# Performance work log

Hardware: AMD Instinct MI355X
Metric: run time of the kernel (lower is better)

## Reference

```python
import jax, jax.numpy as jnp
import numpy as np

N, E = 20000, 320000
NODE_DIM, EDGE_DIM, EMB, HEADS, HIDDEN, OUT = 128, 16, 128, 4, 512, 64
NEG_SLOPE = 0.2


def _gatv2(x, src0, dst0, ea, Wl, bl, Wr, br, We, att, bias):
    """PyG GATv2Conv (concat=True, add_self_loops=True, fill_value='mean')."""
    n = x.shape[0]
    e = src0.shape[0]
    H, C = att.shape
    # self loops; self-loop edge_attr = mean of incoming edge_attr per node (0 if none)
    cnt = jax.ops.segment_sum(jnp.ones((e,), x.dtype), dst0, num_segments=n)
    loop_attr = jax.ops.segment_sum(ea, dst0, num_segments=n) / jnp.maximum(cnt, 1.0)[:, None]
    loops = jnp.arange(n, dtype=src0.dtype)
    src = jnp.concatenate([src0, loops])
    dst = jnp.concatenate([dst0, loops])
    ea_full = jnp.concatenate([ea, loop_attr], axis=0)
    xl = (x @ Wl + bl).reshape(n, H, C)   # source transform
    xr = (x @ Wr + br).reshape(n, H, C)   # target transform
    ef = (ea_full @ We).reshape(-1, H, C)  # edge transform (no bias in PyG)
    s = jax.nn.leaky_relu(xl[src] + xr[dst] + ef, NEG_SLOPE)  # [E', H, C]
    logits = jnp.einsum('ehc,hc->eh', s, att)
    # scatter-softmax over incoming edges of each dst node (stable)
    mx = jax.ops.segment_max(logits, dst, num_segments=n)
    num = jnp.exp(logits - mx[dst])
    den = jax.ops.segment_sum(num, dst, num_segments=n)
    alpha = num / (den[dst] + 1e-16)
    out = jax.ops.segment_sum(alpha[:, :, None] * xl[src], dst, num_segments=n)
    return out.reshape(n, H * C) + bias


def _lin(key, fan_in, fan_out, dt=jnp.float32):
    return jax.random.normal(key, (fan_in, fan_out), dt) * (1.0 / np.sqrt(fan_in))


def setup_inputs() -> dict:
    key = jax.random.key(0)
    ks = jax.random.split(key, 24)
    HC = HEADS * EMB
    inp = {
        'x': jax.random.normal(ks[0], (N, NODE_DIM), jnp.float32),
        'edge_index': jax.random.randint(ks[1], (2, E), 0, N, jnp.int64),
        'edge_attr': jax.random.normal(ks[2], (E, EDGE_DIM), jnp.float32),
        # GATv2 layer 1
        'Wl1': _lin(ks[3], NODE_DIM, HC), 'bl1': jnp.zeros((HC,), jnp.float32),
        'Wr1': _lin(ks[4], NODE_DIM, HC), 'br1': jnp.zeros((HC,), jnp.float32),
        'We1': _lin(ks[5], EDGE_DIM, HC),
        'att1': jax.random.normal(ks[6], (HEADS, EMB), jnp.float32) * (1.0 / np.sqrt(EMB)),
        'bias1': jnp.zeros((HC,), jnp.float32),
        # GATv2 layer 2
        'Wl2': _lin(ks[7], HC, HC), 'bl2': jnp.zeros((HC,), jnp.float32),
        'Wr2': _lin(ks[8], HC, HC), 'br2': jnp.zeros((HC,), jnp.float32),
        'We2': _lin(ks[9], EDGE_DIM, HC),
        'att2': jax.random.normal(ks[10], (HEADS, EMB), jnp.float32) * (1.0 / np.sqrt(EMB)),
        'bias2': jnp.zeros((HC,), jnp.float32),
        # decoder MLP
        'Wd1': _lin(ks[11], HC, HIDDEN), 'bd1': jnp.zeros((HIDDEN,), jnp.float32),
        'Wd2': _lin(ks[12], HIDDEN, OUT), 'bd2': jnp.zeros((OUT,), jnp.float32),
    }
    return inp


def reference(x, edge_index, edge_attr,
              Wl1, bl1, Wr1, br1, We1, att1, bias1,
              Wl2, bl2, Wr2, br2, We2, att2, bias2,
              Wd1, bd1, Wd2, bd2):
    src, dst = edge_index[0], edge_index[1]
    h = _gatv2(x, src, dst, edge_attr, Wl1, bl1, Wr1, br1, We1, att1, bias1)
    h = _gatv2(h, src, dst, edge_attr, Wl2, bl2, Wr2, br2, We2, att2, bias2)
    q = jax.nn.relu(h @ Wd1 + bd1) @ Wd2 + bd2
    return q
```

## Files before the change

### kernel.cpp

```cpp
#include <hip/hip_runtime.h>
#include <hip/hip_fp16.h>

typedef _Float16 half8 __attribute__((ext_vector_type(8)));
typedef _Float16 half4 __attribute__((ext_vector_type(4)));
typedef _Float16 half2v __attribute__((ext_vector_type(2)));
typedef float f32x4 __attribute__((ext_vector_type(4)));

#if __has_builtin(__builtin_amdgcn_fdot2)
#define FDOT2(a, b, c) __builtin_amdgcn_fdot2((a), (b), (c), false)
#else
static __device__ __forceinline__ float FDOT2(half2v a, half2v b, float c) {
  return (float)a[0] * (float)b[0] + (float)a[1] * (float)b[1] + c;
}
#endif
#define H2(v8, p) ((half2v){(v8)[2 * (p)], (v8)[2 * (p) + 1]})

#define GLOAD_LDS16(gp, lp)                                                        \
  __builtin_amdgcn_global_load_lds(                                                \
      (const __attribute__((address_space(1))) void*)(gp),                         \
      (__attribute__((address_space(3))) void*)(lp), 16, 0, 0)

template <int CTRL>
__device__ __forceinline__ float dpp_add16(float x) {
  int y = __builtin_amdgcn_update_dpp(0, __float_as_int(x), CTRL, 0xf, 0xf, true);
  return x + __int_as_float(y);
}
__device__ __forceinline__ float rowsum16(float x) {
  x = dpp_add16<0x128>(x);
  x = dpp_add16<0x124>(x);
  x = dpp_add16<0x122>(x);
  x = dpp_add16<0x121>(x);
  return x;
}

__device__ __forceinline__ int xcd_remap(int bid, int nwg) {
  int xcd = bid & 7, idx = bid >> 3;
  int q8 = nwg >> 3, r8 = nwg & 7;
  return (xcd < r8) ? (xcd * (q8 + 1) + idx)
                    : (r8 * (q8 + 1) + (xcd - r8) * q8 + idx);
}

__global__ void prep_kernel(const float* __restrict__ x, _Float16* __restrict__ x16, int nx,
                            const float* __restrict__ Wl1, const float* __restrict__ Wr1,
                            _Float16* __restrict__ WlrT1,
                            const float* __restrict__ Wl2, const float* __restrict__ Wr2,
                            _Float16* __restrict__ WlrT2,
                            const float* __restrict__ Wd1, _Float16* __restrict__ WdT1,
                            const float* __restrict__ Wd2, _Float16* __restrict__ WdT2,
                            const float* __restrict__ We1, _Float16* __restrict__ WeF1,
                            const float* __restrict__ We2, _Float16* __restrict__ WeF2,
                            const float* __restrict__ att1, _Float16* __restrict__ att16_1,
                            const float* __restrict__ att2, _Float16* __restrict__ att16_2,
                            const int* __restrict__ dst0, int* __restrict__ deg, int E) {
  int i = blockIdx.x * 256 + threadIdx.x;
  if (i < nx) { x16[i] = (_Float16)x[i]; return; }
  i -= nx;
  if (i < 1024 * 128) {
    int n = i >> 7, k = i & 127;
    float v = (n < 512) ? Wl1[(size_t)k * 512 + n] : Wr1[(size_t)k * 512 + (n - 512)];
    WlrT1[i] = (_Float16)v; return;
  }
  i -= 1024 * 128;
  if (i < 1024 * 512) {
    int n = i >> 9, k = i & 511;
    float v = (n < 512) ? Wl2[(size_t)k * 512 + n] : Wr2[(size_t)k * 512 + (n - 512)];
    WlrT2[i] = (_Float16)v; return;
  }
  i -= 1024 * 512;
  if (i < 512 * 512) { int n = i >> 9, k = i & 511; WdT1[i] = (_Float16)Wd1[(size_t)k * 512 + n]; return; }
  i -= 512 * 512;
  if (i < 64 * 512)  { int n = i >> 9, k = i & 511; WdT2[i] = (_Float16)Wd2[(size_t)k * 64 + n]; return; }
  i -= 64 * 512;
  if (i < 512 * 16) {
    int k = i & 15, c = (i >> 4) & 15, g = i >> 8;
    WeF1[i] = (_Float16)We1[(size_t)k * 512 + g * 16 + c]; return;
  }
  i -= 512 * 16;
  if (i < 512 * 16) {
    int k = i & 15, c = (i >> 4) & 15, g = i >> 8;
    WeF2[i] = (_Float16)We2[(size_t)k * 512 + g * 16 + c]; return;
  }
  i -= 512 * 16;
  if (i < 512)       { att16_1[i] = (_Float16)att1[i]; return; }
  i -= 512;
  if (i < 512)       { att16_2[i] = (_Float16)att2[i]; return; }
  i -= 512;
  if (i < E)         { atomicAdd(&deg[dst0[i]], 1); return; }
}

__global__ __launch_bounds__(1024) void scan_kernel(const int* __restrict__ deg, int* __restrict__ offs, int N) {
  __shared__ int part[1024];
  int t = threadIdx.x;
  int chunk = (N + 1023) / 1024;
  int b = t * chunk, e = min(b + chunk, N);
  int s = 0;
  for (int i = b; i < e; i++) s += deg[i] + 1;
  part[t] = s;
  __syncthreads();
  for (int off = 1; off < 1024; off <<= 1) {
    int v = (t >= off) ? part[t - off] : 0;
    __syncthreads();
    part[t] += v;
    __syncthreads();
  }
  int run = (t == 0) ? 0 : part[t - 1];
  for (int i = b; i < e; i++) { offs[i] = run; run += deg[i] + 1; }
  if (t == 1023) offs[N] = part[1023];
}

__global__ void csr_fill_kernel(const int* __restrict__ src0, const int* __restrict__ dst0,
                                const float* __restrict__ ea,
                                const int* __restrict__ offs, const int* __restrict__ deg,
                                int* __restrict__ cnt, int* __restrict__ csr_src,
                                _Float16* __restrict__ eas, int E, int N) {
  int i = blockIdx.x * 256 + threadIdx.x;
  if (i < 64) {
    if (i < 16) csr_src[E + N + i] = 0;
#pragma unroll
    for (int k = 0; k < 16; k++) eas[(size_t)(E + N + i) * 16 + k] = (_Float16)0.f;
  }
  if (i < E) {
    int d = dst0[i];
    int p = offs[d] + atomicAdd(&cnt[d], 1);
    csr_src[p] = src0[i];
    const float* s = ea + (size_t)i * 16;
    half8 h0, h1;
#pragma unroll
    for (int k = 0; k < 8; k++) { h0[k] = (_Float16)s[k]; h1[k] = (_Float16)s[k + 8]; }
    *(half8*)(eas + (size_t)p * 16) = h0;
    *(half8*)(eas + (size_t)p * 16 + 8) = h1;
  } else if (i < E + N) {
    int v = i - E;
    csr_src[offs[v] + deg[v]] = v;
  }
}

__global__ void loop_attr_kernel(const int* __restrict__ offs, const int* __restrict__ deg,
                                 _Float16* __restrict__ eas, int N) {
  int wid = (blockIdx.x * 256 + threadIdx.x) >> 6;
  int l = threadIdx.x & 63;
  if (wid >= N) return;
  int b = offs[wid], dg = deg[wid];
  int k = l & 15, r = l >> 4;
  float s = 0.f;
  for (int j = r; j < dg; j += 4)
    s += (float)eas[(size_t)(b + j) * 16 + k];
  s += __shfl_xor(s, 16, 64);
  s += __shfl_xor(s, 32, 64);
  if (r == 0) eas[(size_t)(b + dg) * 16 + k] = (_Float16)(s / fmaxf((float)dg, 1.0f));
}

template <bool RELU, bool OUT_F32>
__global__ __launch_bounds__(256) void gemm_f16(const _Float16* __restrict__ A,
                                                const _Float16* __restrict__ BT,
                                                const float* __restrict__ biasA,
                                                const float* __restrict__ biasB,
                                                void* __restrict__ CA,
                                                void* __restrict__ CB,
                                                int M, int K, int Nfull, int ldc) {
  __shared__ _Float16 SBUF[4 * 64 * 64];
  _Float16* As = SBUF;
  _Float16* Bs = SBUF + 4096;
  int t = threadIdx.x;
  int gx = gridDim.x, gy = gridDim.y;
  int nwg = gx * gy;
  int bid2 = xcd_remap(blockIdx.y * gx + blockIdx.x, nwg);
  int m0 = (bid2 / gy) * 128;
  int n0 = (bid2 % gy) * 128;
  int l = t & 63, w = t >> 6;
  int wm = w & 1, wn = w >> 1;
  int lr = l & 15, lq = l >> 4;

  f32x4 acc[4][4];
#pragma unroll
  for (int i = 0; i < 4; i++)
#pragma unroll
    for (int j = 0; j < 4; j++) acc[i][j] = (f32x4){0.f, 0.f, 0.f, 0.f};

  int r0 = w * 32 + (l >> 2);
  int cb = (l & 3) * 8;
  const _Float16* Ap = A + (size_t)(m0 + r0) * K + cb;
  const _Float16* Bp = BT + (size_t)(n0 + r0) * K + cb;
  _Float16* AsW = As + w * 32 * 32;
  _Float16* BsW = Bs + w * 32 * 32;

  for (int kk = 0; kk < K; kk += 32) {
    GLOAD_LDS16(Ap, AsW);
    GLOAD_LDS16(Ap + (size_t)16 * K, AsW + 16 * 32);
    GLOAD_LDS16(Bp, BsW);
    GLOAD_LDS16(Bp + (size_t)16 * K, BsW + 16 * 32);
    Ap += 32; Bp += 32;
    __syncthreads();
    half8 af[4], bf[4];
#pragma unroll
    for (int mi = 0; mi < 4; mi++) af[mi] = *(const half8*)&As[(wm * 64 + mi * 16 + lr) * 32 + lq * 8];
#pragma unroll
    for (int ni = 0; ni < 4; ni++) bf[ni] = *(const half8*)&Bs[(wn * 64 + ni * 16 + lr) * 32 + lq * 8];
#pragma unroll
    for (int mi = 0; mi < 4; mi++)
#pragma unroll
      for (int ni = 0; ni < 4; ni++)
        acc[mi][ni] = __builtin_amdgcn_mfma_f32_16x16x32_f16(af[mi], bf[ni], acc[mi][ni], 0, 0, 0);
    __syncthreads();
  }

  if (!OUT_F32) {
    int colbase = n0 + wn * 64;
    const float* biasP = (colbase < 512) ? biasA : biasB;
    int cb0 = (colbase < 512) ? colbase : colbase - 512;
    _Float16* Cx = (_Float16*)((colbase < 512) ? CA : CB);
    _Float16* Cw = SBUF + w * 4096;
#pragma unroll
    for (int ni = 0; ni < 4; ni++) {
      float bv = biasP[cb0 + ni * 16 + lr];
#pragma unroll
      for (int mi = 0; mi < 4; mi++) {
#pragma unroll
        for (int r = 0; r < 4; r++) {
          float v = acc[mi][ni][r] + bv;
          if (RELU) v = fmaxf(v, 0.f);
          Cw[(mi * 16 + lq * 4 + r) * 64 + ni * 16 + lr] = (_Float16)v;
        }
      }
    }
    __syncthreads();
    int lrow = l >> 3, lcb = (l & 7) * 8;
#pragma unroll
    for (int ps = 0; ps < 8; ps++) {
      int row = m0 + wm * 64 + ps * 8 + lrow;
      half8 vv = *(const half8*)(Cw + (ps * 8 + lrow) * 64 + lcb);
      if (row < M) *(half8*)(Cx + (size_t)row * ldc + cb0 + lcb) = vv;
    }
  } else {
#pragma unroll
    for (int ni = 0; ni < 4; ni++) {
      int col = n0 + wn * 64 + ni * 16 + lr;
      if (col >= Nfull) continue;
      float bv = (col < 512) ? biasA[col] : biasB[col - 512];
      float* Cx = (float*)((col < 512) ? CA : CB);
      int cc = (col < 512) ? col : col - 512;
#pragma unroll
      for (int mi = 0; mi < 4; mi++) {
#pragma unroll
        for (int r = 0; r < 4; r++) {
          int row = m0 + wm * 64 + mi * 16 + lq * 4 + r;
          if (row >= M) continue;
          float v = acc[mi][ni][r] + bv;
          if (RELU) v = fmaxf(v, 0.f);
          Cx[(size_t)row * ldc + cc] = v;
        }
      }
    }
  }
}


__device__ __forceinline__ void upd(float p, half8 xs, float& m, float& den, float acc[8]) {
  float mn = fmaxf(m, p);
  float sc = __expf(m - mn);
  float al = __expf(p - mn);
  den = den * sc + al;
#pragma unroll
  for (int jj = 0; jj < 8; jj++) acc[jj] = acc[jj] * sc + al * (float)xs[jj];
  m = mn;
}

__global__ __launch_bounds__(256) void gat_fused_kernel(
    const _Float16* __restrict__ xl,
    const _Float16* __restrict__ xr,
    const int* __restrict__ csr_src, const int* __restrict__ offs,
    const _Float16* __restrict__ eas,
    const _Float16* __restrict__ WeF,
    const _Float16* __restrict__ att16,
    const float* __restrict__ bias,
    _Float16* __restrict__ hout, int N) {
  __shared__ _Float16 WeFL[16 * 512];
  __shared__ _Float16 EFs[4][16 * 512];
  int t = threadIdx.x;
  int l = t & 63;
  int w = t >> 6;
  int h = l >> 4;
  int c0 = l * 8;
  int lr = l & 15, lq = l >> 4;

  {
    const _Float16* gW = WeF + w * 512 + l * 8;
    _Float16* lW = WeFL + w * 512;
#pragma unroll
    for (int p = 0; p < 4; p++) GLOAD_LDS16(gW + p * 2048, lW + p * 2048);
  }
  __syncthreads();

  _Float16* EFw = &EFs[w][0];
  half8 attv = *(const half8*)(att16 + h * 128 + lr * 8);
  const half2v lk = {(_Float16)0.2f, (_Float16)0.2f};

  int wid = blockIdx.x * 4 + w;
  int nw = gridDim.x * 4;

  for (int v0 = wid; v0 < N; v0 += nw) {
    int v = __builtin_amdgcn_readfirstlane(v0);
    int b = offs[v], e2 = offs[v + 1];
    half8 xrv = *(const half8*)(xr + (size_t)v * 512 + c0);

    int s0 = csr_src[b], s1 = csr_src[b + 1], s2 = csr_src[b + 2], s3 = csr_src[b + 3];
    half8 xs0 = *(const half8*)(xl + (size_t)s0 * 512 + c0);
    half8 xs1 = *(const half8*)(xl + (size_t)s1 * 512 + c0);
    half8 xs2 = *(const half8*)(xl + (size_t)s2 * 512 + c0);
    half8 xs3 = *(const half8*)(xl + (size_t)s3 * 512 + c0);
    int t0 = csr_src[b + 4], t1 = csr_src[b + 5], t2 = csr_src[b + 6], t3 = csr_src[b + 7];
    half4 bfrag = *(const half4*)(eas + (size_t)(b + lr) * 16 + lq * 4);

    float m = -1e30f, den = 0.f;
    float acc[8];
#pragma unroll
    for (int j = 0; j < 8; j++) acc[j] = 0.f;

    for (int cs = b; cs < e2; cs += 16) {
#pragma unroll
      for (int g = 0; g < 32; g++) {
        half4 af = *(const half4*)(WeFL + g * 256 + lr * 16 + lq * 4);
        f32x4 d = __builtin_amdgcn_mfma_f32_16x16x16f16(af, bfrag, (f32x4){0.f, 0.f, 0.f, 0.f}, 0, 0, 0);
        half4 hd = {(_Float16)d[0], (_Float16)d[1], (_Float16)d[2], (_Float16)d[3]};
        int hi = (lr * 512 + g * 16 + lq * 4) ^ ((lr & 7) << 3);
        *(half4*)(EFw + hi) = hd;
      }
      bfrag = *(const half4*)(eas + (size_t)(cs + 16 + lr) * 16 + lq * 4);

      int cse = min(cs + 16, e2);
      for (int j = cs; j < cse; j += 4) {
        half8 nx0 = *(const half8*)(xl + (size_t)t0 * 512 + c0);
        half8 nx1 = *(const half8*)(xl + (size_t)t1 * 512 + c0);
        half8 nx2 = *(const half8*)(xl + (size_t)t2 * 512 + c0);
        half8 nx3 = *(const half8*)(xl + (size_t)t3 * 512 + c0);
        int u0 = csr_src[j + 8], u1 = csr_src[j + 9], u2 = csr_src[j + 10], u3 = csr_src[j + 11];

        int si = j - cs;
        half8 ef0 = *(const half8*)(EFw + (((si    ) * 512 + l * 8) ^ (((si    ) & 7) << 3)));
        half8 ef1 = *(const half8*)(EFw + (((si + 1) * 512 + l * 8) ^ (((si + 1) & 7) << 3)));
        half8 ef2 = *(const half8*)(EFw + (((si + 2) * 512 + l * 8) ^ (((si + 2) & 7) << 3)));
        half8 ef3 = *(const half8*)(EFw + (((si + 3) * 512 + l * 8) ^ (((si + 3) & 7) << 3)));

        float p0 = 0.f, p1 = 0.f, p2 = 0.f, p3 = 0.f;
#pragma unroll
        for (int p = 0; p < 4; p++) {
          half2v xrp = H2(xrv, p);
          half2v ap = H2(attv, p);
          half2v v0v = H2(xs0, p) + xrp + H2(ef0, p);
          half2v v1v = H2(xs1, p) + xrp + H2(ef1, p);
          half2v v2v = H2(xs2, p) + xrp + H2(ef2, p);
          half2v v3v = H2(xs3, p) + xrp + H2(ef3, p);
          v0v = __builtin_elementwise_max(v0v, v0v * lk);
          v1v = __builtin_elementwise_max(v1v, v1v * lk);
          v2v = __builtin_elementwise_max(v2v, v2v * lk);
          v3v = __builtin_elementwise_max(v3v, v3v * lk);
          p0 = FDOT2(v0v, ap, p0);
          p1 = FDOT2(v1v, ap, p1);
          p2 = FDOT2(v2v, ap, p2);
          p3 = FDOT2(v3v, ap, p3);
        }
        p0 = rowsum16(p0); p1 = rowsum16(p1); p2 = rowsum16(p2); p3 = rowsum16(p3);

        upd(p0, xs0, m, den, acc);
        if (j + 1 < e2) upd(p1, xs1, m, den, acc);
        if (j + 2 < e2) upd(p2, xs2, m, den, acc);
        if (j + 3 < e2) upd(p3, xs3, m, den, acc);

        xs0 = nx0; xs1 = nx1; xs2 = nx2; xs3 = nx3;
        t0 = u0; t1 = u1; t2 = u2; t3 = u3;
      }
    }
    float rd = 1.f / (den + 1e-16f);
    half8 o;
#pragma unroll
    for (int jj = 0; jj < 8; jj++) o[jj] = (_Float16)(fmaf(acc[jj], rd, bias[c0 + jj]));
    *(half8*)(hout + (size_t)v * 512 + c0) = o;
  }
}


extern "C" void kernel_launch(void* const* d_in, const int* in_sizes, int n_in,
                              void* d_out, int out_size, void* d_ws, size_t ws_size,
                              hipStream_t stream) {
  (void)n_in; (void)out_size; (void)ws_size;
  const float* x    = (const float*)d_in[0];
  const int*   ei   = (const int*)d_in[1];
  const float* ea   = (const float*)d_in[2];
  const float* Wl1  = (const float*)d_in[3];
  const float* bl1  = (const float*)d_in[4];
  const float* Wr1  = (const float*)d_in[5];
  const float* br1  = (const float*)d_in[6];
  const float* We1  = (const float*)d_in[7];
  const float* att1 = (const float*)d_in[8];
  const float* bias1= (const float*)d_in[9];
  const float* Wl2  = (const float*)d_in[10];
  const float* bl2  = (const float*)d_in[11];
  const float* Wr2  = (const float*)d_in[12];
  const float* br2  = (const float*)d_in[13];
  const float* We2  = (const float*)d_in[14];
  const float* att2 = (const float*)d_in[15];
  const float* bias2= (const float*)d_in[16];
  const float* Wd1  = (const float*)d_in[17];
  const float* bd1  = (const float*)d_in[18];
  const float* Wd2  = (const float*)d_in[19];
  const float* bd2  = (const float*)d_in[20];

  const int N = in_sizes[0] / 128;
  const int E = in_sizes[1] / 2;
  const int EP = E + N;
  const int Npad = (N + 127) & ~127;
  const int* src0 = ei;
  const int* dst0 = ei + E;

  char* ws = (char*)d_ws;
  size_t off = 0;
  auto alloc = [&](size_t bytes) -> void* {
    void* p = ws + off;
    off += (bytes + 255) & ~(size_t)255;
    return p;
  };

  int*   deg    = (int*)alloc((size_t)N * 8);
  int*   cnt    = deg + N;
  int*   offs   = (int*)alloc(((size_t)N + 1) * 4);
  int*   csr_src= (int*)alloc(((size_t)EP + 16) * 4);
  _Float16* eas = (_Float16*)alloc(((size_t)EP + 64) * 16 * 2);
  _Float16* x16   = (_Float16*)alloc((size_t)Npad * 128 * 2);
  _Float16* xl16  = (_Float16*)alloc((size_t)Npad * 512 * 2);
  _Float16* xr16  = (_Float16*)alloc((size_t)Npad * 512 * 2);
  _Float16* h16   = (_Float16*)alloc((size_t)Npad * 512 * 2);
  _Float16* WlrT1 = (_Float16*)alloc(1024 * 128 * 2);
  _Float16* WlrT2 = (_Float16*)alloc(1024 * 512 * 2);
  _Float16* WdT1  = (_Float16*)alloc(512 * 512 * 2);
  _Float16* WdT2  = (_Float16*)alloc(128 * 512 * 2);
  _Float16* WeF1  = (_Float16*)alloc(16 * 512 * 2);
  _Float16* WeF2  = (_Float16*)alloc(16 * 512 * 2);
  _Float16* att16_1 = (_Float16*)alloc(512 * 2);
  _Float16* att16_2 = (_Float16*)alloc(512 * 2);
  _Float16* t16   = xl16;

  hipMemsetAsync(deg, 0, (size_t)N * 8, stream);

  int nx = N * 128;
  int prep_base = nx + 1024 * 128 + 1024 * 512 + 512 * 512 + 64 * 512
                + 512 * 16 + 512 * 16 + 512 + 512;
  int prep_total = prep_base + E;
  prep_kernel<<<(prep_total + 255) / 256, 256, 0, stream>>>(
      x, x16, nx, Wl1, Wr1, WlrT1, Wl2, Wr2, WlrT2,
      Wd1, WdT1, Wd2, WdT2, We1, WeF1, We2, WeF2,
      att1, att16_1, att2, att16_2, dst0, deg, E);

  int g;
  scan_kernel<<<1, 1024, 0, stream>>>(deg, offs, N);
  g = (EP + 255) / 256;
  csr_fill_kernel<<<g, 256, 0, stream>>>(src0, dst0, ea, offs, deg, cnt, csr_src, eas, E, N);
  g = (N * 64 + 255) / 256;
  loop_attr_kernel<<<g, 256, 0, stream>>>(offs, deg, eas, N);

  dim3 gb(256);
  dim3 ggm((N + 127) / 128, 8);
  dim3 ggd((N + 127) / 128, 4);
  dim3 ggo((N + 127) / 128, 1);

  const int FGRID = 2048;

  gemm_f16<false, false><<<ggm, gb, 0, stream>>>(x16, WlrT1, bl1, br1, xl16, xr16, N, 128, 1024, 512);
  gat_fused_kernel<<<FGRID, 256, 0, stream>>>(xl16, xr16, csr_src, offs, eas, WeF1, att16_1, bias1, h16, N);

  gemm_f16<false, false><<<ggm, gb, 0, stream>>>(h16, WlrT2, bl2, br2, xl16, xr16, N, 512, 1024, 512);
  gat_fused_kernel<<<FGRID, 256, 0, stream>>>(xl16, xr16, csr_src, offs, eas, WeF2, att16_2, bias2, h16, N);

  gemm_f16<true, false><<<ggd, gb, 0, stream>>>(h16, WdT1, bd1, bd1, t16, t16, N, 512, 512, 512);
  gemm_f16<false, true><<<ggo, gb, 0, stream>>>(t16, WdT2, bd2, bd2, d_out, d_out, N, 512, 64, 64);
}
```

Measured before the change: 450.5 us.

## Split-K the final decoder GEMM with a separate partial-sum reduction kernel

The final 512->64 decoder GEMM previously ran on 157 workgroups with a 128x128 tile, three quarters of which was wasted because only 64 columns exist. It is now a dedicated kernel that splits K into four 128-wide chunks, giving four times as many workgroups with a 128x64 tile, and writes fp32 partial sums into the reused xr16 buffer. A small reduction kernel then adds the four partials plus the bias. This raises parallelism on the small GEMM at the cost of an extra launch and extra global traffic for the partials.

New measurement: 462.3 us. 1.03x slower.

```diff
diff --git a/kernel.cpp b/kernel.cpp
--- a/kernel.cpp
+++ b/kernel.cpp
@@ -150,7 +150,7 @@
   if (r == 0) eas[(size_t)(b + dg) * 16 + k] = (_Float16)(s / fmaxf((float)dg, 1.0f));
 }
 
-template <bool RELU, bool OUT_F32>
+template <bool RELU>
 __global__ __launch_bounds__(256) void gemm_f16(const _Float16* __restrict__ A,
                                                 const _Float16* __restrict__ BT,
                                                 const float* __restrict__ biasA,
@@ -204,54 +204,104 @@
     __syncthreads();
   }
 
-  if (!OUT_F32) {
-    int colbase = n0 + wn * 64;
-    const float* biasP = (colbase < 512) ? biasA : biasB;
-    int cb0 = (colbase < 512) ? colbase : colbase - 512;
-    _Float16* Cx = (_Float16*)((colbase < 512) ? CA : CB);
-    _Float16* Cw = SBUF + w * 4096;
-#pragma unroll
-    for (int ni = 0; ni < 4; ni++) {
-      float bv = biasP[cb0 + ni * 16 + lr];
-#pragma unroll
-      for (int mi = 0; mi < 4; mi++) {
-#pragma unroll
-        for (int r = 0; r < 4; r++) {
-          float v = acc[mi][ni][r] + bv;
-          if (RELU) v = fmaxf(v, 0.f);
-          Cw[(mi * 16 + lq * 4 + r) * 64 + ni * 16 + lr] = (_Float16)v;
-        }
+  int colbase = n0 + wn * 64;
+  const float* biasP = (colbase < 512) ? biasA : biasB;
+  int cb0 = (colbase < 512) ? colbase : colbase - 512;
+  _Float16* Cx = (_Float16*)((colbase < 512) ? CA : CB);
+  _Float16* Cw = SBUF + w * 4096;
+#pragma unroll
+  for (int ni = 0; ni < 4; ni++) {
+    float bv = biasP[cb0 + ni * 16 + lr];
+#pragma unroll
+    for (int mi = 0; mi < 4; mi++) {
+#pragma unroll
+      for (int r = 0; r < 4; r++) {
+        float v = acc[mi][ni][r] + bv;
+        if (RELU) v = fmaxf(v, 0.f);
+        Cw[(mi * 16 + lq * 4 + r) * 64 + ni * 16 + lr] = (_Float16)v;
       }
     }
+  }
+  __syncthreads();
+  int lrow = l >> 3, lcb = (l & 7) * 8;
+#pragma unroll
+  for (int ps = 0; ps < 8; ps++) {
+    int row = m0 + wm * 64 + ps * 8 + lrow;
+    half8 vv = *(const half8*)(Cw + (ps * 8 + lrow) * 64 + lcb);
+    if (row < M) *(half8*)(Cx + (size_t)row * ldc + cb0 + lcb) = vv;
+  }
+}
+
+__global__ __launch_bounds__(256) void gemm_dec2(const _Float16* __restrict__ A,
+                                                 const _Float16* __restrict__ BT,
+                                                 float* __restrict__ qpart,
+                                                 int M, int lda) {
+  __shared__ _Float16 As[128 * 32];
+  __shared__ _Float16 Bs[64 * 32];
+  int t = threadIdx.x;
+  int gy = 4;
+  int nwg = gridDim.x * gy;
+  int bid2 = xcd_remap(blockIdx.y * gridDim.x + blockIdx.x, nwg);
+  int m0 = (bid2 / gy) * 128;
+  int s  = bid2 % gy;
+  int kb = s * 128;
+  int l = t & 63, w = t >> 6;
+  int lr = l & 15, lq = l >> 4;
+
+  f32x4 acc[2][4];
+#pragma unroll
+  for (int i = 0; i < 2; i++)
+#pragma unroll
+    for (int j = 0; j < 4; j++) acc[i][j] = (f32x4){0.f, 0.f, 0.f, 0.f};
+
+  int r0 = w * 32 + (l >> 2);
+  int rb = w * 16 + (l >> 2);
+  int cb = (l & 3) * 8;
+  const _Float16* Ap = A + (size_t)(m0 + r0) * lda + kb + cb;
+  const _Float16* Bp = BT + (size_t)rb * lda + kb + cb;
+  _Float16* AsW = As + w * 32 * 32;
+  _Float16* BsW = Bs + w * 16 * 32;
+
+  for (int kk = 0; kk < 128; kk += 32) {
+    GLOAD_LDS16(Ap, AsW);
+    GLOAD_LDS16(Ap + (size_t)16 * lda, AsW + 16 * 32);
+    GLOAD_LDS16(Bp, BsW);
+    Ap += 32; Bp += 32;
     __syncthreads();
-    int lrow = l >> 3, lcb = (l & 7) * 8;
-#pragma unroll
-    for (int ps = 0; ps < 8; ps++) {
-      int row = m0 + wm * 64 + ps * 8 + lrow;
-      half8 vv = *(const half8*)(Cw + (ps * 8 + lrow) * 64 + lcb);
-      if (row < M) *(half8*)(Cx + (size_t)row * ldc + cb0 + lcb) = vv;
-    }
-  } else {
-#pragma unroll
-    for (int ni = 0; ni < 4; ni++) {
-      int col = n0 + wn * 64 + ni * 16 + lr;
-      if (col >= Nfull) continue;
-      float bv = (col < 512) ? biasA[col] : biasB[col - 512];
-      float* Cx = (float*)((col < 512) ? CA : CB);
-      int cc = (col < 512) ? col : col - 512;
-#pragma unroll
-      for (int mi = 0; mi < 4; mi++) {
-#pragma unroll
-        for (int r = 0; r < 4; r++) {
-          int row = m0 + wm * 64 + mi * 16 + lq * 4 + r;
-          if (row >= M) continue;
-          float v = acc[mi][ni][r] + bv;
-          if (RELU) v = fmaxf(v, 0.f);
-          Cx[(size_t)row * ldc + cc] = v;
-        }
+    half8 af[2], bf[4];
+#pragma unroll
+    for (int mi = 0; mi < 2; mi++) af[mi] = *(const half8*)&As[(w * 32 + mi * 16 + lr) * 32 + lq * 8];
+#pragma unroll
+    for (int ni = 0; ni < 4; ni++) bf[ni] = *(const half8*)&Bs[(ni * 16 + lr) * 32 + lq * 8];
+#pragma unroll
+    for (int mi = 0; mi < 2; mi++)
+#pragma unroll
+      for (int ni = 0; ni < 4; ni++)
+        acc[mi][ni] = __builtin_amdgcn_mfma_f32_16x16x32_f16(af[mi], bf[ni], acc[mi][ni], 0, 0, 0);
+    __syncthreads();
+  }
+
+  float* qp = qpart + (size_t)s * M * 64;
+#pragma unroll
+  for (int ni = 0; ni < 4; ni++) {
+    int col = ni * 16 + lr;
+#pragma unroll
+    for (int mi = 0; mi < 2; mi++) {
+#pragma unroll
+      for (int r = 0; r < 4; r++) {
+        int row = m0 + w * 32 + mi * 16 + lq * 4 + r;
+        if (row < M) qp[(size_t)row * 64 + col] = acc[mi][ni][r];
       }
     }
   }
+}
+
+__global__ void dec2_reduce(const float* __restrict__ qp, const float* __restrict__ bd2,
+                            float* __restrict__ q, int n) {
+  int i = blockIdx.x * 256 + threadIdx.x;
+  if (i >= n) return;
+  float s = (qp[i] + qp[i + (size_t)n]) + (qp[i + 2 * (size_t)n] + qp[i + 3 * (size_t)n]);
+  q[i] = s + bd2[i & 63];
 }
 
 
@@ -438,6 +488,7 @@
   _Float16* att16_1 = (_Float16*)alloc(512 * 2);
   _Float16* att16_2 = (_Float16*)alloc(512 * 2);
   _Float16* t16   = xl16;
+  float* qpart    = (float*)xr16;
 
   hipMemsetAsync(deg, 0, (size_t)N * 8, stream);
 
@@ -460,16 +511,17 @@
   dim3 gb(256);
   dim3 ggm((N + 127) / 128, 8);
   dim3 ggd((N + 127) / 128, 4);
-  dim3 ggo((N + 127) / 128, 1);
+  dim3 gg2((N + 127) / 128, 4);
 
   const int FGRID = 2048;
 
-  gemm_f16<false, false><<<ggm, gb, 0, stream>>>(x16, WlrT1, bl1, br1, xl16, xr16, N, 128, 1024, 512);
+  gemm_f16<false><<<ggm, gb, 0, stream>>>(x16, WlrT1, bl1, br1, xl16, xr16, N, 128, 1024, 512);
   gat_fused_kernel<<<FGRID, 256, 0, stream>>>(xl16, xr16, csr_src, offs, eas, WeF1, att16_1, bias1, h16, N);
 
-  gemm_f16<false, false><<<ggm, gb, 0, stream>>>(h16, WlrT2, bl2, br2, xl16, xr16, N, 512, 1024, 512);
+  gemm_f16<false><<<ggm, gb, 0, stream>>>(h16, WlrT2, bl2, br2, xl16, xr16, N, 512, 1024, 512);
   gat_fused_kernel<<<FGRID, 256, 0, stream>>>(xl16, xr16, csr_src, offs, eas, WeF2, att16_2, bias2, h16, N);
 
-  gemm_f16<true, false><<<ggd, gb, 0, stream>>>(h16, WdT1, bd1, bd1, t16, t16, N, 512, 512, 512);
-  gemm_f16<false, true><<<ggo, gb, 0, stream>>>(t16, WdT2, bd2, bd2, d_out, d_out, N, 512, 64, 64);
-}
+  gemm_f16<true><<<ggd, gb, 0, stream>>>(h16, WdT1, bd1, bd1, t16, t16, N, 512, 512, 512);
+  gemm_dec2<<<gg2, gb, 0, stream>>>(t16, WdT2, qpart, N, 512);
+  dec2_reduce<<<(N * 64 + 255) / 256, 256, 0, stream>>>(qpart, bd2, (float*)d_out, N * 64);
+}
```
